# Optimization experiments

Measured on AMD Instinct MI355X. Metric: run time of the kernel, lower is better.

The kernel has to match this reference:

```python
import jax, jax.numpy as jnp
import numpy as np

N_EMBED = 1024
N_HEADS = 16
HEAD_DIM = N_EMBED // N_HEADS


def setup_inputs() -> dict:
    key = jax.random.key(0)
    ks = jax.random.split(key, 5)
    x = jax.random.normal(ks[0], (4, 2048, N_EMBED), dtype=jnp.float32)
    # Linear params (torch nn.Linear: y = x @ W.T + b); store W as [in, out]
    s = 1.0 / np.sqrt(N_EMBED)
    W_attn = jax.random.uniform(ks[1], (N_EMBED, 3 * N_EMBED), minval=-s, maxval=s, dtype=jnp.float32)
    b_attn = jax.random.uniform(ks[2], (3 * N_EMBED,), minval=-s, maxval=s, dtype=jnp.float32)
    W_proj = jax.random.uniform(ks[3], (N_EMBED, N_EMBED), minval=-s, maxval=s, dtype=jnp.float32)
    b_proj = jax.random.uniform(ks[4], (N_EMBED,), minval=-s, maxval=s, dtype=jnp.float32)
    return {"x": x, "W_attn": W_attn, "b_attn": b_attn, "W_proj": W_proj, "b_proj": b_proj}


def reference(x, W_attn, b_attn, W_proj, b_proj):
    B, L, D = x.shape
    H, Hd = N_HEADS, HEAD_DIM
    qkv = x @ W_attn + b_attn  # [B, L, 3D]
    q, k, v = jnp.split(qkv, 3, axis=-1)
    q = q.reshape(B, L, H, Hd).transpose(0, 2, 1, 3)  # [B, H, L, Hd]
    k = k.reshape(B, L, H, Hd).transpose(0, 2, 1, 3)
    v = v.reshape(B, L, H, Hd).transpose(0, 2, 1, 3)
    scores = jnp.einsum('bhqd,bhkd->bhqk', q, k) / jnp.sqrt(jnp.float32(Hd))
    causal = jnp.tril(jnp.ones((L, L), dtype=bool))
    scores = jnp.where(causal[None, None], scores, -jnp.inf)
    probs = jax.nn.softmax(scores.astype(jnp.float32), axis=-1).astype(x.dtype)
    o = jnp.einsum('bhqk,bhkd->bhqd', probs, v)  # [B, H, L, Hd]
    o = o.transpose(0, 2, 1, 3).reshape(B, L, D)
    return o @ W_proj + b_proj
```

## Files before the change

### kernel.cpp

```cpp
#include <hip/hip_runtime.h>


typedef __attribute__((ext_vector_type(8))) short short8;
typedef __attribute__((ext_vector_type(4))) short s16x4;
typedef __attribute__((ext_vector_type(4))) float f32x4;

#define DEVI __device__ __forceinline__

constexpr int NE = 1024, NH = 16, NB = 4, L = 2048;
constexpr int M = NB * L;
constexpr int KD = 1024;

DEVI unsigned f2bf(float f) {
    union { float f; unsigned u; } v; v.f = f;
    unsigned u = v.u;
    u += 0x7fffu + ((u >> 16) & 1u);
    return u >> 16;
}
DEVI unsigned pack_bf2(float lo, float hi) {
    union { float f; unsigned u; } a, b; a.f = lo; b.f = hi;
    return ((a.u + 0x8000u) >> 16) | ((b.u + 0x8000u) & 0xffff0000u);
}

typedef const __attribute__((address_space(1))) void* gas_t;
typedef __attribute__((address_space(3))) void* las_t;
DEVI void gl_lds16(const void* g, void* l) {
    __builtin_amdgcn_global_load_lds((gas_t)g, (las_t)l, 16, 0, 0);
}

__global__ void k_f32_to_bf16(const float* __restrict__ in,
                              unsigned short* __restrict__ out, int n8) {
    int i = blockIdx.x * blockDim.x + threadIdx.x;
    if (i >= n8) return;
    const float4* p = (const float4*)in + (size_t)i * 2;
    float4 a = p[0], b = p[1];
    short8 r;
    r[0] = f2bf(a.x); r[1] = f2bf(a.y); r[2] = f2bf(a.z); r[3] = f2bf(a.w);
    r[4] = f2bf(b.x); r[5] = f2bf(b.y); r[6] = f2bf(b.z); r[7] = f2bf(b.w);
    ((short8*)out)[i] = r;
}

__global__ void k_transpose_bf16(const float* __restrict__ in,
                                 unsigned short* __restrict__ out, int R, int C) {
    __shared__ float t[32][33];
    int x = blockIdx.x * 32 + threadIdx.x;
    int y0 = blockIdx.y * 32;
#pragma unroll
    for (int i = 0; i < 4; i++)
        t[threadIdx.y + 8 * i][threadIdx.x] = in[(size_t)(y0 + threadIdx.y + 8 * i) * C + x];
    __syncthreads();
    int xo = y0 + threadIdx.x;
    int yo = blockIdx.x * 32 + threadIdx.y;
#pragma unroll
    for (int i = 0; i < 4; i++)
        out[(size_t)(yo + 8 * i) * R + xo] = f2bf(t[threadIdx.x][threadIdx.y + 8 * i]);
}


#define PH_SYNC                                                      \
    __builtin_amdgcn_s_barrier();                                    \
    asm volatile("s_waitcnt lgkmcnt(0)" ::: "memory");               \
    __builtin_amdgcn_sched_barrier(0);

#define RD_A(ROFF, SWZ)                                              \
    _Pragma("unroll") for (int mt = 0; mt < 4; mt++)                 \
        af[mt] = *(const short8*)&aCur[((ROFF) + mt * 16 + l16) * 64 + (SWZ)];

#define RD_B(BF, SWZ)                                                \
    _Pragma("unroll") for (int nt = 0; nt < NF; nt++)                \
        BF[nt] = *(const short8*)&bCur[(bro + nt * 16 + l16) * 64 + (SWZ)];

#define MFMA_CLU(MH4, BF)                                            \
    __builtin_amdgcn_s_setprio(1);                                   \
    _Pragma("unroll") for (int mt = 0; mt < 4; mt++)                 \
    _Pragma("unroll") for (int nt = 0; nt < NF; nt++)                \
        acc[(MH4) + mt][nt] = __builtin_amdgcn_mfma_f32_16x16x32_bf16( \
            af[mt], BF[nt], acc[(MH4) + mt][nt], 0, 0, 0);           \
    __builtin_amdgcn_s_setprio(0);

#define GTILE(KT, CA, CA2, PAR, DOPRE)                               \
  {                                                                  \
    const short* aCur = &As3[(CA) * 16384 + wg_m * 8192];            \
    const short* bCur = &Bs[(PAR) * (BN * 64)];                      \
                                             \
    RD_A(0, swz0)                                                    \
    RD_B(bf0, swz0)                                                  \
    if (DOPRE) stA((KT) + 2, 0, (CA2));                              \
    PH_SYNC                                                          \
    MFMA_CLU(0, bf0)                                                 \
    __builtin_amdgcn_s_barrier();                                    \
                                             \
    RD_A(64, swz0)                                                   \
    if (DOPRE) stA((KT) + 2, 1, (CA2));                              \
    PH_SYNC                                                          \
    MFMA_CLU(4, bf0)                                                 \
    __builtin_amdgcn_s_barrier();                                    \
                                             \
    RD_A(0, swz1)                                                    \
    RD_B(bf1, swz1)                                                  \
    PH_SYNC                                                          \
    MFMA_CLU(0, bf1)                                                 \
    __builtin_amdgcn_s_barrier();                                    \
                                             \
    RD_A(64, swz1)                                                   \
    if (DOPRE) { stB((KT) + 2, 0, (PAR)); stB((KT) + 2, 1, (PAR)); } \
    PH_SYNC                                                          \
    MFMA_CLU(4, bf1)                                                 \
    if (DOPRE) {                                                     \
        if (MODE == 0) asm volatile("s_waitcnt vmcnt(8)" ::: "memory"); \
        else           asm volatile("s_waitcnt vmcnt(6)" ::: "memory"); \
    } else {                                                         \
        asm volatile("s_waitcnt vmcnt(0)" ::: "memory");             \
    }                                                                \
    __builtin_amdgcn_s_barrier();                                    \
  }

template <int MODE>
__global__ __launch_bounds__(512, 2)
void k_gemm8(const unsigned short* __restrict__ A,
             const unsigned short* __restrict__ Bt,
             const float* __restrict__ bias,
             unsigned short* __restrict__ Qb,
             unsigned short* __restrict__ Kb,
             unsigned short* __restrict__ Vt,
             float* __restrict__ out) {
    constexpr int BN  = (MODE == 0) ? 256 : 128;
    constexpr int NF  = BN / 64;
    constexpr int NBN = (MODE == 0) ? 12 : 8;
    constexpr int NWG = (MODE == 0) ? 384 : 256;
    constexpr int NT  = KD / 64;

    __shared__ alignas(16) short As3[3 * 2 * 128 * 64];
    __shared__ alignas(16) short Bs[2 * BN * 64];

    const int tid = threadIdx.x;
    const int lane = tid & 63, wid = tid >> 6;
    const int quad = lane >> 4, l16 = lane & 15;
    const int wg_m = wid >> 2, wg_n = wid & 3;

    const int id = ((int)blockIdx.x & 7) * (NWG >> 3) + ((int)blockIdx.x >> 3);
    const int mb = id / NBN, nb = id - mb * NBN;
    const int m0 = mb * 256, n0 = nb * BN;

    const int srow = lane >> 3;
    const int gcol = ((lane & 7) ^ srow) * 8;

    const unsigned short* Ag = A + (size_t)m0 * KD + gcol;
    const unsigned short* Bg = Bt + (size_t)n0 * KD + gcol;

    auto stA = [&](int kt, int h, int reg) {
#pragma unroll
        for (int c = 0; c < 2; c++) {
            const int rb = wid * 16 + c * 8;
            gl_lds16(Ag + (size_t)(h * 128 + rb + srow) * KD + kt * 64,
                     &As3[reg * 16384 + h * 8192 + rb * 64]);
        }
    };
    auto stB = [&](int kt, int h, int reg) {
#pragma unroll
        for (int c = 0; c < BN / 128; c++) {
            const int rb = wid * (BN / 128) * 8 + c * 8;
            gl_lds16(Bg + (size_t)(h * (BN / 2) + rb + srow) * KD + kt * 64,
                     &Bs[reg * (BN * 64) + h * (BN / 2) * 64 + rb * 64]);
        }
    };

    const int swz0 = ((quad) ^ (l16 & 7)) * 8;
    const int swz1 = ((4 + quad) ^ (l16 & 7)) * 8;
    const int bro = wg_n * (BN / 4);

    f32x4 acc[8][NF] = {};
    short8 af[4], bf0[NF], bf1[NF];

    stA(0, 0, 0); stA(0, 1, 0);
    stB(0, 0, 0); stB(0, 1, 0);
    stA(1, 0, 1); stA(1, 1, 1);
    stB(1, 0, 1); stB(1, 1, 1);
    if (MODE == 0) asm volatile("s_waitcnt vmcnt(8)" ::: "memory");
    else           asm volatile("s_waitcnt vmcnt(6)" ::: "memory");
    __builtin_amdgcn_s_barrier();

    int ca = 0;
    for (int kt = 0; kt < NT - 2; kt++) {
        const int ca2 = (ca >= 1) ? ca - 1 : 2;
        const int par = kt & 1;
        GTILE(kt, ca, ca2, par, 1)
        ca = (ca >= 2) ? 0 : ca + 1;
    }
    GTILE(NT - 2, ca, 0, ((NT - 2) & 1), 0)
    ca = (ca >= 2) ? 0 : ca + 1;
    GTILE(NT - 1, ca, 0, ((NT - 1) & 1), 0)

#pragma unroll
    for (int nt = 0; nt < NF; nt++) {
        const int n = n0 + wg_n * (BN / 4) + nt * 16 + l16;
        const float bv = bias[n];
        if (MODE == 0) {
            const int sel = n >> 10;
            const int h = (n & 1023) >> 6;
            const int d = n & 63;
#pragma unroll
            for (int mt = 0; mt < 8; mt++)
#pragma unroll
                for (int r = 0; r < 4; r++) {
                    const int m = m0 + wg_m * 128 + mt * 16 + quad * 4 + r;
                    const int b = m >> 11, l = m & 2047;
                    const int bh = b * NH + h;
                    const float v = acc[mt][nt][r] + bv;
                    if (sel == 0)      Qb[(size_t)(bh * L + l) * 64 + d] = f2bf(v * 0.125f);
                    else if (sel == 1) Kb[(size_t)(bh * L + l) * 64 + d] = f2bf(v);
                    else               Vt[(size_t)(bh * 64 + d) * L + l] = f2bf(v);
                }
        } else {
#pragma unroll
            for (int mt = 0; mt < 8; mt++)
#pragma unroll
                for (int r = 0; r < 4; r++) {
                    const int m = m0 + wg_m * 128 + mt * 16 + quad * 4 + r;
                    out[(size_t)m * NE + n] = acc[mt][nt][r] + bv;
                }
        }
    }
}

__global__ __launch_bounds__(256, 4)
void k_attn(const unsigned short* __restrict__ Q,
            const unsigned short* __restrict__ Kb,
            const unsigned short* __restrict__ Vt,
            unsigned short* __restrict__ O) {
    __shared__ alignas(16) short smem[16384];
    short* Ks = smem;
    short* Vs = smem + 8192;
    short* Os = smem;

    const int tid = threadIdx.x;
    const int lane = tid & 63, wid = tid >> 6;
    const int quad = lane >> 4, l16 = lane & 15;
    const int bh = blockIdx.x;
    const int qb = 15 - (int)blockIdx.y;
    const int q0 = qb * 128 + wid * 32;
    const size_t base = (size_t)bh * L * 64;
    const int b = bh >> 4, h = bh & 15;

    const int srowK = lane >> 3;
    const int gsegK = (lane & 7) ^ srowK;
    const int vrow_off = (lane >> 4);
    const int vseg = lane & 15;

    short8 qf[2][2];
#pragma unroll
    for (int mt = 0; mt < 2; mt++)
#pragma unroll
        for (int dc = 0; dc < 2; dc++)
            qf[mt][dc] = *(const short8*)&Q[base + (size_t)(q0 + mt * 16 + l16) * 64 + dc * 32 + quad * 8];

    f32x4 o[2][4] = {};
    float lrow[2] = {0.f, 0.f};

    for (int kt = 0; kt <= qb; kt++) {
        __syncthreads();
#pragma unroll
        for (int c = 0; c < 4; c++) {
            const int rbase = c * 32 + wid * 8;
            gl_lds16(&Kb[base + (size_t)(kt * 128 + rbase + srowK) * 64 + gsegK * 8],
                     &Ks[rbase * 64]);
        }
#pragma unroll
        for (int c = 0; c < 4; c++) {
            const int rbase = c * 16 + wid * 4;
            const int row = rbase + vrow_off;
            const int gs = vseg ^ (row & 15);
            gl_lds16(&Vt[base + (size_t)row * L + kt * 128 + gs * 8], &Vs[rbase * 128]);
        }
        __syncthreads();

        const bool diag = (kt == qb);
        const int chunks = diag ? (wid + 1) : 4;

        for (int kc = 0; kc < chunks; kc++) {
            short8 kf[2][2];
#pragma unroll
            for (int j0 = 0; j0 < 2; j0++)
#pragma unroll
                for (int dc = 0; dc < 2; dc++) {
                    const int R = kc * 32 + j0 * 16 + l16;
                    kf[j0][dc] = *(const short8*)&Ks[R * 64 + (((dc * 4 + quad) ^ (R & 7)) * 8)];
                }
            f32x4 st[2][2];
#pragma unroll
            for (int mt = 0; mt < 2; mt++)
#pragma unroll
                for (int j0 = 0; j0 < 2; j0++) {
                    f32x4 z = {};
                    z = __builtin_amdgcn_mfma_f32_16x16x32_bf16(kf[j0][0], qf[mt][0], z, 0, 0, 0);
                    z = __builtin_amdgcn_mfma_f32_16x16x32_bf16(kf[j0][1], qf[mt][1], z, 0, 0, 0);
                    st[mt][j0] = z;
                }
            const bool dm = diag && (kc == wid);
            short8 pb[2];
#pragma unroll
            for (int mt = 0; mt < 2; mt++) {
                float pe[8];
                float sum = 0.f;
#pragma unroll
                for (int j0 = 0; j0 < 2; j0++)
#pragma unroll
                    for (int r = 0; r < 4; r++) {
                        float p = __expf(st[mt][j0][r]);
                        if (dm) {
                            const int krel = j0 * 16 + quad * 4 + r;
                            const int qrel = mt * 16 + l16;
                            if (krel > qrel) p = 0.f;
                        }
                        sum += p;
                        pe[j0 * 4 + r] = p;
                    }
                lrow[mt] += sum;
#pragma unroll
                for (int w = 0; w < 4; w++) {
                    unsigned pk = pack_bf2(pe[2 * w], pe[2 * w + 1]);
                    pb[mt][2 * w] = (short)(pk & 0xffff);
                    pb[mt][2 * w + 1] = (short)(pk >> 16);
                }
            }
#pragma unroll
            for (int dt = 0; dt < 4; dt++) {
                const int R2 = dt * 16 + l16;
                const int s16a = kc * 4 + (quad >> 1);
                const int off = (quad & 1) * 4;
                s16x4 lo = *(const s16x4*)&Vs[R2 * 128 + ((s16a ^ l16) * 8) + off];
                s16x4 hi = *(const s16x4*)&Vs[R2 * 128 + (((s16a + 2) ^ l16) * 8) + off];
                short8 vf = __builtin_shufflevector(lo, hi, 0, 1, 2, 3, 4, 5, 6, 7);
#pragma unroll
                for (int mt = 0; mt < 2; mt++)
                    o[mt][dt] = __builtin_amdgcn_mfma_f32_16x16x32_bf16(
                        vf, pb[mt], o[mt][dt], 0, 0, 0);
            }
        }
    }

    float inv[2];
#pragma unroll
    for (int mt = 0; mt < 2; mt++) {
        float rs = lrow[mt];
        rs += __shfl_xor(rs, 16);
        rs += __shfl_xor(rs, 32);
        inv[mt] = 1.0f / rs;
    }

    __syncthreads();
#pragma unroll
    for (int mt = 0; mt < 2; mt++) {
        const int ql = wid * 32 + mt * 16 + l16;
#pragma unroll
        for (int dt = 0; dt < 4; dt++) {
            unsigned w0 = f2bf(o[mt][dt][0] * inv[mt]) | (f2bf(o[mt][dt][1] * inv[mt]) << 16);
            unsigned w1 = f2bf(o[mt][dt][2] * inv[mt]) | (f2bf(o[mt][dt][3] * inv[mt]) << 16);
            *(uint2*)&Os[ql * 72 + dt * 16 + quad * 4] = make_uint2(w0, w1);
        }
    }
    __syncthreads();
#pragma unroll
    for (int i = 0; i < 4; i++) {
        const int id = i * 256 + tid;
        const int row = id >> 3, seg = id & 7;
        short8 v = *(const short8*)&Os[row * 72 + seg * 8];
        const int q = qb * 128 + row;
        *(short8*)&O[(size_t)(b * L + q) * NE + h * 64 + seg * 8] = v;
    }
}

extern "C" void kernel_launch(void* const* d_in, const int* in_sizes, int n_in,
                              void* d_out, int out_size, void* d_ws, size_t ws_size,
                              hipStream_t stream) {
    const float* x  = (const float*)d_in[0];
    const float* Wa = (const float*)d_in[1];
    const float* ba = (const float*)d_in[2];
    const float* Wp = (const float*)d_in[3];
    const float* bp = (const float*)d_in[4];
    float* out = (float*)d_out;

    char* ws = (char*)d_ws;
    unsigned short* xb  = (unsigned short*)(ws);
    unsigned short* WaT = (unsigned short*)(ws + (16u << 20));
    unsigned short* WpT = (unsigned short*)(ws + (22u << 20));
    unsigned short* Qb  = (unsigned short*)(ws + (24u << 20));
    unsigned short* Kb  = (unsigned short*)(ws + (40u << 20));
    unsigned short* Vt  = (unsigned short*)(ws + (56u << 20));

    k_f32_to_bf16<<<(M * NE / 8 + 255) / 256, 256, 0, stream>>>(x, xb, M * NE / 8);
    k_transpose_bf16<<<dim3(3 * NE / 32, NE / 32), dim3(32, 8), 0, stream>>>(Wa, WaT, NE, 3 * NE);
    k_transpose_bf16<<<dim3(NE / 32, NE / 32), dim3(32, 8), 0, stream>>>(Wp, WpT, NE, NE);

    k_gemm8<0><<<dim3(384), 512, 0, stream>>>(xb, WaT, ba, Qb, Kb, Vt, nullptr);

    unsigned short* Ob = xb;
    k_attn<<<dim3(NB * NH, 16), 256, 0, stream>>>(Qb, Kb, Vt, Ob);

    k_gemm8<1><<<dim3(256), 512, 0, stream>>>(Ob, WpT, bp, nullptr, nullptr, nullptr, out);
}
```

Baseline: 271.1 us.

## Retile QKV GEMM to 256x192 tiles and drop per-phase LDS waits

The QKV projection GEMM now uses a 256x192 output tile instead of 256x256, which gives 512 workgroups instead of 384. The B-tile staging is restructured around this shape, and the vmcnt wait counts are adjusted to match the new number of loads in flight. The explicit lgkmcnt(0) wait and sched_barrier after each phase barrier are removed, leaving the compiler to place its own waits on LDS reads. The intent is better occupancy and load balance across CUs with less barrier stall time. The cost is lower data reuse per tile and a risk to the LDS ordering that the removed waits used to guarantee.

```diff
diff --git a/kernel.cpp b/kernel.cpp
--- a/kernel.cpp
+++ b/kernel.cpp
@@ -57,11 +57,6 @@
 }
 
 
-#define PH_SYNC                                                      \
-    __builtin_amdgcn_s_barrier();                                    \
-    asm volatile("s_waitcnt lgkmcnt(0)" ::: "memory");               \
-    __builtin_amdgcn_sched_barrier(0);
-
 #define RD_A(ROFF, SWZ)                                              \
     _Pragma("unroll") for (int mt = 0; mt < 4; mt++)                 \
         af[mt] = *(const short8*)&aCur[((ROFF) + mt * 16 + l16) * 64 + (SWZ)];
@@ -77,6 +72,10 @@
         acc[(MH4) + mt][nt] = __builtin_amdgcn_mfma_f32_16x16x32_bf16( \
             af[mt], BF[nt], acc[(MH4) + mt][nt], 0, 0, 0);           \
     __builtin_amdgcn_s_setprio(0);
+
+#define VM_WAIT_STEADY                                               \
+    if (MODE == 0) asm volatile("s_waitcnt vmcnt(7)" ::: "memory");  \
+    else           asm volatile("s_waitcnt vmcnt(6)" ::: "memory");
 
 #define GTILE(KT, CA, CA2, PAR, DOPRE)                               \
   {                                                                  \
@@ -86,32 +85,28 @@
     RD_A(0, swz0)                                                    \
     RD_B(bf0, swz0)                                                  \
     if (DOPRE) stA((KT) + 2, 0, (CA2));                              \
-    PH_SYNC                                                          \
+    __builtin_amdgcn_s_barrier();                                    \
     MFMA_CLU(0, bf0)                                                 \
     __builtin_amdgcn_s_barrier();                                    \
                                              \
     RD_A(64, swz0)                                                   \
     if (DOPRE) stA((KT) + 2, 1, (CA2));                              \
-    PH_SYNC                                                          \
+    __builtin_amdgcn_s_barrier();                                    \
     MFMA_CLU(4, bf0)                                                 \
     __builtin_amdgcn_s_barrier();                                    \
                                              \
     RD_A(0, swz1)                                                    \
     RD_B(bf1, swz1)                                                  \
-    PH_SYNC                                                          \
+    __builtin_amdgcn_s_barrier();                                    \
     MFMA_CLU(0, bf1)                                                 \
     __builtin_amdgcn_s_barrier();                                    \
-                                             \
+     \
     RD_A(64, swz1)                                                   \
-    if (DOPRE) { stB((KT) + 2, 0, (PAR)); stB((KT) + 2, 1, (PAR)); } \
-    PH_SYNC                                                          \
+    if (DOPRE) stB((KT) + 2, (PAR));                                 \
+    __builtin_amdgcn_s_barrier();                                    \
     MFMA_CLU(4, bf1)                                                 \
-    if (DOPRE) {                                                     \
-        if (MODE == 0) asm volatile("s_waitcnt vmcnt(8)" ::: "memory"); \
-        else           asm volatile("s_waitcnt vmcnt(6)" ::: "memory"); \
-    } else {                                                         \
-        asm volatile("s_waitcnt vmcnt(0)" ::: "memory");             \
-    }                                                                \
+    if (DOPRE) { VM_WAIT_STEADY }                                    \
+    else       { asm volatile("s_waitcnt vmcnt(0)" ::: "memory"); }  \
     __builtin_amdgcn_s_barrier();                                    \
   }
 
@@ -124,11 +119,12 @@
              unsigned short* __restrict__ Kb,
              unsigned short* __restrict__ Vt,
              float* __restrict__ out) {
-    constexpr int BN  = (MODE == 0) ? 256 : 128;
+    constexpr int BN  = (MODE == 0) ? 192 : 128;
     constexpr int NF  = BN / 64;
-    constexpr int NBN = (MODE == 0) ? 12 : 8;
-    constexpr int NWG = (MODE == 0) ? 384 : 256;
+    constexpr int NBN = (MODE == 0) ? 16 : 8;
+    constexpr int NWG = (MODE == 0) ? 512 : 256;
     constexpr int NT  = KD / 64;
+    constexpr int CHB = BN / 64;
 
     __shared__ alignas(16) short As3[3 * 2 * 128 * 64];
     __shared__ alignas(16) short Bs[2 * BN * 64];
@@ -156,12 +152,12 @@
                      &As3[reg * 16384 + h * 8192 + rb * 64]);
         }
     };
-    auto stB = [&](int kt, int h, int reg) {
-#pragma unroll
-        for (int c = 0; c < BN / 128; c++) {
-            const int rb = wid * (BN / 128) * 8 + c * 8;
-            gl_lds16(Bg + (size_t)(h * (BN / 2) + rb + srow) * KD + kt * 64,
-                     &Bs[reg * (BN * 64) + h * (BN / 2) * 64 + rb * 64]);
+    auto stB = [&](int kt, int reg) {
+#pragma unroll
+        for (int c = 0; c < CHB; c++) {
+            const int rb = (c * 8 + wid) * 8;
+            gl_lds16(Bg + (size_t)(rb + srow) * KD + kt * 64,
+                     &Bs[reg * (BN * 64) + rb * 64]);
         }
     };
 
@@ -172,12 +168,9 @@
     f32x4 acc[8][NF] = {};
     short8 af[4], bf0[NF], bf1[NF];
 
-    stA(0, 0, 0); stA(0, 1, 0);
-    stB(0, 0, 0); stB(0, 1, 0);
-    stA(1, 0, 1); stA(1, 1, 1);
-    stB(1, 0, 1); stB(1, 1, 1);
-    if (MODE == 0) asm volatile("s_waitcnt vmcnt(8)" ::: "memory");
-    else           asm volatile("s_waitcnt vmcnt(6)" ::: "memory");
+    stA(0, 0, 0); stA(0, 1, 0); stB(0, 0);
+    stA(1, 0, 1); stA(1, 1, 1); stB(1, 1);
+    VM_WAIT_STEADY
     __builtin_amdgcn_s_barrier();
 
     int ca = 0;
@@ -392,7 +385,7 @@
     k_transpose_bf16<<<dim3(3 * NE / 32, NE / 32), dim3(32, 8), 0, stream>>>(Wa, WaT, NE, 3 * NE);
     k_transpose_bf16<<<dim3(NE / 32, NE / 32), dim3(32, 8), 0, stream>>>(Wp, WpT, NE, NE);
 
-    k_gemm8<0><<<dim3(384), 512, 0, stream>>>(xb, WaT, ba, Qb, Kb, Vt, nullptr);
+    k_gemm8<0><<<dim3(512), 512, 0, stream>>>(xb, WaT, ba, Qb, Kb, Vt, nullptr);
 
     unsigned short* Ob = xb;
     k_attn<<<dim3(NB * NH, 16), 256, 0, stream>>>(Qb, Kb, Vt, Ob);
```

New measurement: 272.8 us. About the same (+0.6%).
